# Optimization experiments

Hardware: AMD Instinct MI355X
Metric: run time of the kernel (lower is better)

Reference implementation:

```python
import jax, jax.numpy as jnp
import numpy as np

EMBED_DIM = 1024


def setup_inputs() -> dict:
    key = jax.random.key(0)
    ks = jax.random.split(key, 7)
    B, S, D = 4, 2048, EMBED_DIM
    scale = 1.0 / np.sqrt(D)
    x = jax.random.normal(ks[0], (B, S, D), dtype=jnp.float32)
    # nn.Linear weights stored as [out, in]; we keep [in, out] for x @ W
    Wq = jax.random.normal(ks[1], (D, D), dtype=jnp.float32) * scale
    bq = jax.random.normal(ks[2], (D,), dtype=jnp.float32) * scale
    Wk = jax.random.normal(ks[3], (D, D), dtype=jnp.float32) * scale
    bk = jax.random.normal(ks[4], (D,), dtype=jnp.float32) * scale
    Wv = jax.random.normal(ks[5], (D, D), dtype=jnp.float32) * scale
    bv = jax.random.normal(ks[6], (D,), dtype=jnp.float32) * scale
    return {"x": x, "Wq": Wq, "bq": bq, "Wk": Wk, "bk": bk, "Wv": Wv, "bv": bv}


def reference(x, Wq, bq, Wk, bk, Wv, bv):
    # Single-head attention (num_heads unused in original module).
    q = x @ Wq + bq            # [B, S, D]
    k = x @ Wk + bk            # [B, S, D]
    v = x @ Wv + bv            # [B, S, D]
    inv_sqrt_d = 1.0 / jnp.sqrt(jnp.asarray(x.shape[-1], x.dtype))
    scores = jnp.einsum("bsd,btd->bst", q, k) * inv_sqrt_d  # [B, S, S]
    attn = jax.nn.softmax(scores, axis=-1)
    return jnp.einsum("bst,btd->bsd", attn, v)
```

## Files before the change

kernel.cpp:

```cpp
#include <hip/hip_runtime.h>
#include <hip/hip_bf16.h>


using floatx4 = __attribute__((ext_vector_type(4))) float;
using shortx8 = __attribute__((ext_vector_type(8))) short;
using shortx4 = __attribute__((ext_vector_type(4))) short;

__device__ __forceinline__ short f2bf(float f) {
    __hip_bfloat16 h = __float2bfloat16(f);
    return *reinterpret_cast<short*>(&h);
}
__device__ __forceinline__ float bf2f(short s) {
    unsigned u = (unsigned)(unsigned short)s << 16;
    return __uint_as_float(u);
}

#define MFMA16(a, b, c) __builtin_amdgcn_mfma_f32_16x16x32_bf16((a), (b), (c), 0, 0, 0)

__device__ __forceinline__ void gld_lds16(const void* g, void* l) {
    __builtin_amdgcn_global_load_lds(
        (const __attribute__((address_space(1))) void*)g,
        (__attribute__((address_space(3))) void*)l, 16, 0, 0);
}

__device__ __forceinline__ void gemm_loop(
    const short* __restrict__ A, const short* __restrict__ B,
    size_t lda, size_t ldb, int K,
    short* as_, short* bs_, floatx4 (&acc)[4][4], int w, int l)
{
    const int lr8 = l >> 3;
    const int swz = ((l & 7) ^ lr8) * 8;
    const int lrow = l & 15, quad = l >> 4;
    const int wr = w >> 1, wc = w & 1;
    const int r8r = lrow & 7;
    const short* pa = A + (size_t)(w * 32 + lr8) * lda + swz;
    const short* pb = B + (size_t)(w * 32 + lr8) * ldb + swz;
    short* la = as_ + w * 4 * 512;
    short* lb = bs_ + w * 4 * 512;

    for (int kt = 0; kt < K; kt += 64) {
        for (int c = 0; c < 4; ++c) {
            gld_lds16(pa + (size_t)c * 8 * lda + kt, la + c * 512);
            gld_lds16(pb + (size_t)c * 8 * ldb + kt, lb + c * 512);
        }
        __syncthreads();
        for (int kk = 0; kk < 64; kk += 32) {
            const int xoff = (((kk >> 3) + quad) ^ r8r) << 3;
            shortx8 af[4], bfr[4];
            for (int i = 0; i < 4; ++i)
                af[i] = *reinterpret_cast<const shortx8*>(
                    &as_[(size_t)(wr * 64 + i * 16 + lrow) * 64 + xoff]);
            for (int j = 0; j < 4; ++j)
                bfr[j] = *reinterpret_cast<const shortx8*>(
                    &bs_[(size_t)(wc * 64 + j * 16 + lrow) * 64 + xoff]);
            for (int i = 0; i < 4; ++i)
                for (int j = 0; j < 4; ++j)
                    acc[i][j] = MFMA16(af[i], bfr[j], acc[i][j]);
        }
        __syncthreads();
    }
}

__global__ __launch_bounds__(256) void wconv_kernel(
    const float* __restrict__ Wq, const float* __restrict__ Wk,
    const float* __restrict__ Wv, short* __restrict__ Wt)
{
    const float* src = (blockIdx.z == 0) ? Wq : (blockIdx.z == 1) ? Wk : Wv;
    short* dst = Wt + (size_t)blockIdx.z * 1024 * 1024;
    __shared__ float t[64][65];
    const int k0 = blockIdx.x * 64, n0 = blockIdx.y * 64;
    for (int i = threadIdx.x; i < 64 * 64; i += 256) {
        int r = i >> 6, c = i & 63;
        t[r][c] = src[(size_t)(k0 + r) * 1024 + n0 + c];
    }
    __syncthreads();
    for (int i = threadIdx.x; i < 64 * 64; i += 256) {
        int r = i >> 6, c = i & 63;
        dst[(size_t)(n0 + r) * 1024 + k0 + c] = f2bf(t[c][r]);
    }
}

__global__ __launch_bounds__(256) void xconv_kernel(
    const float* __restrict__ X, short* __restrict__ Xb)
{
    size_t i = ((size_t)blockIdx.x * 256 + threadIdx.x) * 8;
    float4 v0 = *reinterpret_cast<const float4*>(X + i);
    float4 v1 = *reinterpret_cast<const float4*>(X + i + 4);
    shortx8 s;
    s[0] = f2bf(v0.x); s[1] = f2bf(v0.y); s[2] = f2bf(v0.z); s[3] = f2bf(v0.w);
    s[4] = f2bf(v1.x); s[5] = f2bf(v1.y); s[6] = f2bf(v1.z); s[7] = f2bf(v1.w);
    *reinterpret_cast<shortx8*>(Xb + i) = s;
}

__global__ __launch_bounds__(256) void qkv_lds_kernel(
    const short* __restrict__ Xb, const short* __restrict__ Wt,
    const float* __restrict__ bias, short* __restrict__ outN,
    short* __restrict__ outVt, int vmode)
{
    __shared__ short as_[128 * 64];
    __shared__ short bs_[128 * 64];
    const int t = threadIdx.x, w = t >> 6, l = t & 63;
    const int m0 = blockIdx.x * 128, n0 = blockIdx.y * 128;
    const int wr = w >> 1, wc = w & 1, lrow = l & 15, quad = l >> 4;

    floatx4 acc[4][4];
    for (int i = 0; i < 4; ++i)
        for (int j = 0; j < 4; ++j) acc[i][j] = floatx4{0.f, 0.f, 0.f, 0.f};

    gemm_loop(Xb + (size_t)m0 * 1024, Wt + (size_t)n0 * 1024,
              1024, 1024, 1024, as_, bs_, acc, w, l);

    for (int i = 0; i < 4; ++i) {
        int rbase = m0 + wr * 64 + i * 16 + quad * 4;
        for (int j = 0; j < 4; ++j) {
            int col = n0 + wc * 64 + j * 16 + lrow;
            float bv = bias[col];
            if (!vmode) {
                for (int r = 0; r < 4; ++r)
                    outN[(size_t)(rbase + r) * 1024 + col] = f2bf(acc[i][j][r] + bv);
            } else {
                int b = rbase >> 11, sl = rbase & 2047;
                shortx4 s;
                for (int r = 0; r < 4; ++r) s[r] = f2bf(acc[i][j][r] + bv);
                *reinterpret_cast<shortx4*>(&outVt[((size_t)b * 1024 + col) * 2048 + sl]) = s;
            }
        }
    }
}

__global__ __launch_bounds__(256) void qkv_cvt_kernel(
    const float* __restrict__ X, const short* __restrict__ Wt,
    const float* __restrict__ bias, short* __restrict__ outN,
    short* __restrict__ outVt, int vmode)
{
    __shared__ short as_[128 * 64];
    __shared__ short bs_[128 * 64];
    const int t = threadIdx.x, w = t >> 6, l = t & 63;
    const int m0 = blockIdx.x * 128, n0 = blockIdx.y * 128;
    const int wr = w >> 1, wc = w & 1, lrow = l & 15, quad = l >> 4;
    const int r8r = lrow & 7;
    const int lr8 = l >> 3;
    const int swz = ((l & 7) ^ lr8) * 8;
    const short* pb = Wt + (size_t)(n0 + w * 32 + lr8) * 1024 + swz;
    short* lb = bs_ + w * 4 * 512;

    floatx4 acc[4][4];
    for (int i = 0; i < 4; ++i)
        for (int j = 0; j < 4; ++j) acc[i][j] = floatx4{0.f, 0.f, 0.f, 0.f};

    for (int kt = 0; kt < 1024; kt += 64) {
        for (int c = 0; c < 4; ++c)
            gld_lds16(pb + (size_t)c * 8 * 1024 + kt, lb + c * 512);
        for (int i = 0; i < 8; ++i) {
            int fid = t + i * 256;
            int r = fid >> 4, c4 = fid & 15;
            float4 v = *reinterpret_cast<const float4*>(
                &X[(size_t)(m0 + r) * 1024 + kt + c4 * 4]);
            shortx4 s;
            s[0] = f2bf(v.x); s[1] = f2bf(v.y); s[2] = f2bf(v.z); s[3] = f2bf(v.w);
            int pos = ((((c4 >> 1) ^ (r & 7)) << 3) | ((c4 & 1) << 2));
            *reinterpret_cast<shortx4*>(&as_[(size_t)r * 64 + pos]) = s;
        }
        __syncthreads();
        for (int kk = 0; kk < 64; kk += 32) {
            const int xoff = (((kk >> 3) + quad) ^ r8r) << 3;
            shortx8 af[4], bfr[4];
            for (int i = 0; i < 4; ++i)
                af[i] = *reinterpret_cast<const shortx8*>(
                    &as_[(size_t)(wr * 64 + i * 16 + lrow) * 64 + xoff]);
            for (int j = 0; j < 4; ++j)
                bfr[j] = *reinterpret_cast<const shortx8*>(
                    &bs_[(size_t)(wc * 64 + j * 16 + lrow) * 64 + xoff]);
            for (int i = 0; i < 4; ++i)
                for (int j = 0; j < 4; ++j)
                    acc[i][j] = MFMA16(af[i], bfr[j], acc[i][j]);
        }
        __syncthreads();
    }

    for (int i = 0; i < 4; ++i) {
        int rbase = m0 + wr * 64 + i * 16 + quad * 4;
        for (int j = 0; j < 4; ++j) {
            int col = n0 + wc * 64 + j * 16 + lrow;
            float bv = bias[col];
            if (!vmode) {
                for (int r = 0; r < 4; ++r)
                    outN[(size_t)(rbase + r) * 1024 + col] = f2bf(acc[i][j][r] + bv);
            } else {
                int b = rbase >> 11, sl = rbase & 2047;
                shortx4 s;
                for (int r = 0; r < 4; ++r) s[r] = f2bf(acc[i][j][r] + bv);
                *reinterpret_cast<shortx4*>(&outVt[((size_t)b * 1024 + col) * 2048 + sl]) = s;
            }
        }
    }
}

__global__ __launch_bounds__(256) void scores_kernel(
    const short* __restrict__ Qb, const short* __restrict__ Kb,
    short* __restrict__ P, int row_start)
{
    __shared__ short as_[128 * 64];
    __shared__ short bs_[128 * 64];
    const int t = threadIdx.x, w = t >> 6, l = t & 63;
    const int m0 = blockIdx.x * 128;
    const int n0 = blockIdx.y * 128;
    const int g0 = row_start + m0;
    const int b = g0 >> 11;
    const int wr = w >> 1, wc = w & 1, lrow = l & 15, quad = l >> 4;

    floatx4 acc[4][4];
    for (int i = 0; i < 4; ++i)
        for (int j = 0; j < 4; ++j) acc[i][j] = floatx4{0.f, 0.f, 0.f, 0.f};

    gemm_loop(Qb + (size_t)g0 * 1024, Kb + ((size_t)b * 2048 + n0) * 1024,
              1024, 1024, 1024, as_, bs_, acc, w, l);

    for (int i = 0; i < 4; ++i) {
        int rbase = m0 + wr * 64 + i * 16 + quad * 4;
        for (int j = 0; j < 4; ++j) {
            int col = n0 + wc * 64 + j * 16 + lrow;
            for (int r = 0; r < 4; ++r)
                P[(size_t)(rbase + r) * 2048 + col] =
                    f2bf(__expf(acc[i][j][r] * 0.03125f - 20.0f));
        }
    }
}

__global__ __launch_bounds__(256) void rsum_kernel(
    const short* __restrict__ P, float* __restrict__ invs)
{
    const int w = threadIdx.x >> 6, l = threadIdx.x & 63;
    const int row = blockIdx.x * 4 + w;
    const short* pr = P + (size_t)row * 2048;
    float s = 0.f;
    for (int i = 0; i < 4; ++i) {
        shortx8 v = *reinterpret_cast<const shortx8*>(pr + l * 8 + i * 512);
        for (int j = 0; j < 8; ++j) s += bf2f(v[j]);
    }
    for (int m = 32; m >= 1; m >>= 1) s += __shfl_xor(s, m, 64);
    if (l == 0) invs[row] = 1.0f / s;
}

__global__ __launch_bounds__(256) void pv_kernel(
    const short* __restrict__ Pb, const short* __restrict__ Vt,
    const float* __restrict__ invs, float* __restrict__ Out, int row_start)
{
    __shared__ short as_[128 * 64];
    __shared__ short bs_[128 * 64];
    const int t = threadIdx.x, w = t >> 6, l = t & 63;
    const int m0 = blockIdx.x * 128;
    const int n0 = blockIdx.y * 128;
    const int g0 = row_start + m0;
    const int b = g0 >> 11;
    const int wr = w >> 1, wc = w & 1, lrow = l & 15, quad = l >> 4;

    floatx4 acc[4][4];
    for (int i = 0; i < 4; ++i)
        for (int j = 0; j < 4; ++j) acc[i][j] = floatx4{0.f, 0.f, 0.f, 0.f};

    gemm_loop(Pb + (size_t)m0 * 2048, Vt + ((size_t)b * 1024 + n0) * 2048,
              2048, 2048, 2048, as_, bs_, acc, w, l);

    for (int i = 0; i < 4; ++i) {
        int rloc = m0 + wr * 64 + i * 16 + quad * 4;
        int rglb = row_start + rloc;
        float is[4];
        for (int r = 0; r < 4; ++r) is[r] = invs[rloc + r];
        for (int j = 0; j < 4; ++j) {
            int col = n0 + wc * 64 + j * 16 + lrow;
            for (int r = 0; r < 4; ++r)
                Out[(size_t)(rglb + r) * 1024 + col] = acc[i][j][r] * is[r];
        }
    }
}

extern "C" void kernel_launch(void* const* d_in, const int* in_sizes, int n_in,
                              void* d_out, int out_size, void* d_ws, size_t ws_size,
                              hipStream_t stream)
{
    const float* x  = (const float*)d_in[0];
    const float* Wq = (const float*)d_in[1];
    const float* bq = (const float*)d_in[2];
    const float* Wk = (const float*)d_in[3];
    const float* bk = (const float*)d_in[4];
    const float* Wv = (const float*)d_in[5];
    const float* bv = (const float*)d_in[6];
    float* out = (float*)d_out;

    char* ws = (char*)d_ws;
    const size_t WT_B  = (size_t)3 * 1024 * 1024 * 2;
    const size_t QKV_B = (size_t)8192 * 1024 * 2;
    short* Wt = (short*)ws;
    short* Qb = (short*)(ws + WT_B);
    short* Kb = (short*)(ws + WT_B + QKV_B);
    short* Vt = (short*)(ws + WT_B + 2 * QKV_B);
    char*  region = ws + WT_B + 3 * QKV_B;
    const size_t base = WT_B + 3 * QKV_B;

    size_t avail = ws_size > base ? ws_size - base : 0;
    long rows_fit = (long)(avail / (size_t)(2048 * 2 + 4));
    int chunk = (int)(rows_fit & ~127L);
    if (chunk > 8192) chunk = 8192;
    if (chunk < 128) chunk = 128;
    const bool use_xb = avail >= QKV_B;

    short* Pbuf = (short*)region;
    float* invs = (float*)(region + (size_t)chunk * 2048 * 2);

    wconv_kernel<<<dim3(16, 16, 3), 256, 0, stream>>>(Wq, Wk, Wv, Wt);
    if (use_xb) {
        short* Xb = (short*)region;
        xconv_kernel<<<dim3(4096), 256, 0, stream>>>(x, Xb);
        qkv_lds_kernel<<<dim3(64, 8), 256, 0, stream>>>(Xb, Wt,                   bq, Qb, nullptr, 0);
        qkv_lds_kernel<<<dim3(64, 8), 256, 0, stream>>>(Xb, Wt + 1024 * 1024,     bk, Kb, nullptr, 0);
        qkv_lds_kernel<<<dim3(64, 8), 256, 0, stream>>>(Xb, Wt + 2 * 1024 * 1024, bv, nullptr, Vt, 1);
    } else {
        qkv_cvt_kernel<<<dim3(64, 8), 256, 0, stream>>>(x, Wt,                    bq, Qb, nullptr, 0);
        qkv_cvt_kernel<<<dim3(64, 8), 256, 0, stream>>>(x, Wt + 1024 * 1024,      bk, Kb, nullptr, 0);
        qkv_cvt_kernel<<<dim3(64, 8), 256, 0, stream>>>(x, Wt + 2 * 1024 * 1024,  bv, nullptr, Vt, 1);
    }

    for (int rs = 0; rs < 8192; rs += chunk) {
        int rows = 8192 - rs;
        if (rows > chunk) rows = chunk;
        scores_kernel<<<dim3(rows / 128, 16), 256, 0, stream>>>(Qb, Kb, Pbuf, rs);
        rsum_kernel<<<dim3(rows / 4), 256, 0, stream>>>(Pbuf, invs);
        pv_kernel<<<dim3(rows / 128, 8), 256, 0, stream>>>(Pbuf, Vt, invs, out, rs);
    }
}
```

Baseline: 258.0 us.

## Fuse prep and QKV launches, fold softmax row sums into scores kernel

The weight-transpose, x-conversion, bias-concat and sum-zeroing kernels become one prep launch, and the three QKV GEMMs become a single launch over a concatenated N dimension. The separate row-sum kernel is removed: the scores kernel reduces each row's exp values with wave shuffles and accumulates them into a global sums array with atomics. Q and K are now stored in the output buffer to free workspace, and the grid axes are swapped so blocks sharing a row tile are adjacent. This removes several launches and one full re-read of P. In exchange it adds atomic traffic, and it risks corrupting results when chunking overwrites Q and K in the output before later chunks read them.

```diff
diff --git a/kernel.cpp b/kernel.cpp
--- a/kernel.cpp
+++ b/kernel.cpp
@@ -61,47 +61,62 @@
     }
 }
 
-__global__ __launch_bounds__(256) void wconv_kernel(
+__global__ __launch_bounds__(256) void prep_kernel(
+    const float* __restrict__ X,
     const float* __restrict__ Wq, const float* __restrict__ Wk,
-    const float* __restrict__ Wv, short* __restrict__ Wt)
-{
-    const float* src = (blockIdx.z == 0) ? Wq : (blockIdx.z == 1) ? Wk : Wv;
-    short* dst = Wt + (size_t)blockIdx.z * 1024 * 1024;
-    __shared__ float t[64][65];
-    const int k0 = blockIdx.x * 64, n0 = blockIdx.y * 64;
-    for (int i = threadIdx.x; i < 64 * 64; i += 256) {
-        int r = i >> 6, c = i & 63;
-        t[r][c] = src[(size_t)(k0 + r) * 1024 + n0 + c];
-    }
-    __syncthreads();
-    for (int i = threadIdx.x; i < 64 * 64; i += 256) {
-        int r = i >> 6, c = i & 63;
-        dst[(size_t)(n0 + r) * 1024 + k0 + c] = f2bf(t[c][r]);
-    }
-}
-
-__global__ __launch_bounds__(256) void xconv_kernel(
-    const float* __restrict__ X, short* __restrict__ Xb)
-{
-    size_t i = ((size_t)blockIdx.x * 256 + threadIdx.x) * 8;
-    float4 v0 = *reinterpret_cast<const float4*>(X + i);
-    float4 v1 = *reinterpret_cast<const float4*>(X + i + 4);
-    shortx8 s;
-    s[0] = f2bf(v0.x); s[1] = f2bf(v0.y); s[2] = f2bf(v0.z); s[3] = f2bf(v0.w);
-    s[4] = f2bf(v1.x); s[5] = f2bf(v1.y); s[6] = f2bf(v1.z); s[7] = f2bf(v1.w);
-    *reinterpret_cast<shortx8*>(Xb + i) = s;
-}
-
-__global__ __launch_bounds__(256) void qkv_lds_kernel(
+    const float* __restrict__ Wv,
+    const float* __restrict__ bq, const float* __restrict__ bk,
+    const float* __restrict__ bv,
+    short* __restrict__ Xb, short* __restrict__ Wt,
+    float* __restrict__ bcat, float* __restrict__ sums)
+{
+    const int id = blockIdx.x, t = threadIdx.x;
+    if (id < 4096) {
+        size_t i = ((size_t)id * 256 + t) * 8;
+        float4 v0 = *reinterpret_cast<const float4*>(X + i);
+        float4 v1 = *reinterpret_cast<const float4*>(X + i + 4);
+        shortx8 s;
+        s[0] = f2bf(v0.x); s[1] = f2bf(v0.y); s[2] = f2bf(v0.z); s[3] = f2bf(v0.w);
+        s[4] = f2bf(v1.x); s[5] = f2bf(v1.y); s[6] = f2bf(v1.z); s[7] = f2bf(v1.w);
+        *reinterpret_cast<shortx8*>(Xb + i) = s;
+    } else if (id < 4864) {
+        __shared__ float tl[64][65];
+        const int wid = id - 4096;
+        const int z = wid >> 8, t16 = wid & 255;
+        const float* src = (z == 0) ? Wq : (z == 1) ? Wk : Wv;
+        short* dst = Wt + (size_t)z * 1024 * 1024;
+        const int k0 = (t16 >> 4) * 64, n0 = (t16 & 15) * 64;
+        for (int i = t; i < 64 * 64; i += 256) {
+            int r = i >> 6, c = i & 63;
+            tl[r][c] = src[(size_t)(k0 + r) * 1024 + n0 + c];
+        }
+        __syncthreads();
+        for (int i = t; i < 64 * 64; i += 256) {
+            int r = i >> 6, c = i & 63;
+            dst[(size_t)(n0 + r) * 1024 + k0 + c] = f2bf(tl[c][r]);
+        }
+    } else if (id < 4867) {
+        const int z = id - 4864;
+        const float* bsrc = (z == 0) ? bq : (z == 1) ? bk : bv;
+        for (int i = t; i < 1024; i += 256) bcat[z * 1024 + i] = bsrc[i];
+    } else {
+        const int sid = id - 4867;
+        *reinterpret_cast<float4*>(&sums[sid * 1024 + t * 4]) =
+            float4{0.f, 0.f, 0.f, 0.f};
+    }
+}
+
+__global__ __launch_bounds__(256) void qkv_kernel(
     const short* __restrict__ Xb, const short* __restrict__ Wt,
-    const float* __restrict__ bias, short* __restrict__ outN,
-    short* __restrict__ outVt, int vmode)
+    const float* __restrict__ bcat, short* __restrict__ dQ,
+    short* __restrict__ dK, short* __restrict__ Vt)
 {
     __shared__ short as_[128 * 64];
     __shared__ short bs_[128 * 64];
     const int t = threadIdx.x, w = t >> 6, l = t & 63;
-    const int m0 = blockIdx.x * 128, n0 = blockIdx.y * 128;
+    const int n0 = blockIdx.x * 128, m0 = blockIdx.y * 128;
     const int wr = w >> 1, wc = w & 1, lrow = l & 15, quad = l >> 4;
+    const int sec = n0 >> 10;
 
     floatx4 acc[4][4];
     for (int i = 0; i < 4; ++i)
@@ -110,101 +125,75 @@
     gemm_loop(Xb + (size_t)m0 * 1024, Wt + (size_t)n0 * 1024,
               1024, 1024, 1024, as_, bs_, acc, w, l);
 
+    short* outN = (sec == 0) ? dQ : dK;
     for (int i = 0; i < 4; ++i) {
         int rbase = m0 + wr * 64 + i * 16 + quad * 4;
         for (int j = 0; j < 4; ++j) {
-            int col = n0 + wc * 64 + j * 16 + lrow;
-            float bv = bias[col];
-            if (!vmode) {
+            int coln = n0 + wc * 64 + j * 16 + lrow;
+            int col = coln & 1023;
+            float bv = bcat[coln];
+            if (sec < 2) {
                 for (int r = 0; r < 4; ++r)
                     outN[(size_t)(rbase + r) * 1024 + col] = f2bf(acc[i][j][r] + bv);
             } else {
                 int b = rbase >> 11, sl = rbase & 2047;
                 shortx4 s;
                 for (int r = 0; r < 4; ++r) s[r] = f2bf(acc[i][j][r] + bv);
-                *reinterpret_cast<shortx4*>(&outVt[((size_t)b * 1024 + col) * 2048 + sl]) = s;
+                *reinterpret_cast<shortx4*>(&Vt[((size_t)b * 1024 + col) * 2048 + sl]) = s;
             }
         }
     }
 }
 
-__global__ __launch_bounds__(256) void qkv_cvt_kernel(
-    const float* __restrict__ X, const short* __restrict__ Wt,
-    const float* __restrict__ bias, short* __restrict__ outN,
-    short* __restrict__ outVt, int vmode)
+__global__ __launch_bounds__(256) void scores_kernel(
+    const short* __restrict__ dQ, const short* __restrict__ dK,
+    short* __restrict__ P, float* __restrict__ sums, int row_start)
 {
     __shared__ short as_[128 * 64];
     __shared__ short bs_[128 * 64];
     const int t = threadIdx.x, w = t >> 6, l = t & 63;
-    const int m0 = blockIdx.x * 128, n0 = blockIdx.y * 128;
+    const int n0 = blockIdx.x * 128;
+    const int m0 = blockIdx.y * 128;
+    const int g0 = row_start + m0;
+    const int b = g0 >> 11;
     const int wr = w >> 1, wc = w & 1, lrow = l & 15, quad = l >> 4;
-    const int r8r = lrow & 7;
-    const int lr8 = l >> 3;
-    const int swz = ((l & 7) ^ lr8) * 8;
-    const short* pb = Wt + (size_t)(n0 + w * 32 + lr8) * 1024 + swz;
-    short* lb = bs_ + w * 4 * 512;
 
     floatx4 acc[4][4];
     for (int i = 0; i < 4; ++i)
         for (int j = 0; j < 4; ++j) acc[i][j] = floatx4{0.f, 0.f, 0.f, 0.f};
 
-    for (int kt = 0; kt < 1024; kt += 64) {
-        for (int c = 0; c < 4; ++c)
-            gld_lds16(pb + (size_t)c * 8 * 1024 + kt, lb + c * 512);
-        for (int i = 0; i < 8; ++i) {
-            int fid = t + i * 256;
-            int r = fid >> 4, c4 = fid & 15;
-            float4 v = *reinterpret_cast<const float4*>(
-                &X[(size_t)(m0 + r) * 1024 + kt + c4 * 4]);
-            shortx4 s;
-            s[0] = f2bf(v.x); s[1] = f2bf(v.y); s[2] = f2bf(v.z); s[3] = f2bf(v.w);
-            int pos = ((((c4 >> 1) ^ (r & 7)) << 3) | ((c4 & 1) << 2));
-            *reinterpret_cast<shortx4*>(&as_[(size_t)r * 64 + pos]) = s;
-        }
-        __syncthreads();
-        for (int kk = 0; kk < 64; kk += 32) {
-            const int xoff = (((kk >> 3) + quad) ^ r8r) << 3;
-            shortx8 af[4], bfr[4];
-            for (int i = 0; i < 4; ++i)
-                af[i] = *reinterpret_cast<const shortx8*>(
-                    &as_[(size_t)(wr * 64 + i * 16 + lrow) * 64 + xoff]);
-            for (int j = 0; j < 4; ++j)
-                bfr[j] = *reinterpret_cast<const shortx8*>(
-                    &bs_[(size_t)(wc * 64 + j * 16 + lrow) * 64 + xoff]);
-            for (int i = 0; i < 4; ++i)
-                for (int j = 0; j < 4; ++j)
-                    acc[i][j] = MFMA16(af[i], bfr[j], acc[i][j]);
-        }
-        __syncthreads();
-    }
+    gemm_loop(dQ + (size_t)g0 * 1024, dK + ((size_t)b * 2048 + n0) * 1024,
+              1024, 1024, 1024, as_, bs_, acc, w, l);
 
     for (int i = 0; i < 4; ++i) {
-        int rbase = m0 + wr * 64 + i * 16 + quad * 4;
+        int rloc = m0 + wr * 64 + i * 16 + quad * 4;
+        float rs[4] = {0.f, 0.f, 0.f, 0.f};
         for (int j = 0; j < 4; ++j) {
             int col = n0 + wc * 64 + j * 16 + lrow;
-            float bv = bias[col];
-            if (!vmode) {
-                for (int r = 0; r < 4; ++r)
-                    outN[(size_t)(rbase + r) * 1024 + col] = f2bf(acc[i][j][r] + bv);
-            } else {
-                int b = rbase >> 11, sl = rbase & 2047;
-                shortx4 s;
-                for (int r = 0; r < 4; ++r) s[r] = f2bf(acc[i][j][r] + bv);
-                *reinterpret_cast<shortx4*>(&outVt[((size_t)b * 1024 + col) * 2048 + sl]) = s;
+            for (int r = 0; r < 4; ++r) {
+                short pb = f2bf(__expf(acc[i][j][r] * 0.03125f - 20.0f));
+                P[(size_t)(rloc + r) * 2048 + col] = pb;
+                rs[r] += bf2f(pb);
             }
         }
-    }
-}
-
-__global__ __launch_bounds__(256) void scores_kernel(
-    const short* __restrict__ Qb, const short* __restrict__ Kb,
-    short* __restrict__ P, int row_start)
+        for (int r = 0; r < 4; ++r)
+            for (int m = 1; m <= 8; m <<= 1)
+                rs[r] += __shfl_xor(rs[r], m, 64);
+        if (lrow == 0)
+            for (int r = 0; r < 4; ++r)
+                atomicAdd(&sums[row_start + rloc + r], rs[r]);
+    }
+}
+
+__global__ __launch_bounds__(256) void pv_kernel(
+    const short* __restrict__ P, const short* __restrict__ Vt,
+    const float* __restrict__ sums, float* __restrict__ Out, int row_start)
 {
     __shared__ short as_[128 * 64];
     __shared__ short bs_[128 * 64];
     const int t = threadIdx.x, w = t >> 6, l = t & 63;
-    const int m0 = blockIdx.x * 128;
-    const int n0 = blockIdx.y * 128;
+    const int n0 = blockIdx.x * 128;
+    const int m0 = blockIdx.y * 128;
     const int g0 = row_start + m0;
     const int b = g0 >> 11;
     const int wr = w >> 1, wc = w & 1, lrow = l & 15, quad = l >> 4;
@@ -213,60 +202,14 @@
     for (int i = 0; i < 4; ++i)
         for (int j = 0; j < 4; ++j) acc[i][j] = floatx4{0.f, 0.f, 0.f, 0.f};
 
-    gemm_loop(Qb + (size_t)g0 * 1024, Kb + ((size_t)b * 2048 + n0) * 1024,
-              1024, 1024, 1024, as_, bs_, acc, w, l);
-
-    for (int i = 0; i < 4; ++i) {
-        int rbase = m0 + wr * 64 + i * 16 + quad * 4;
-        for (int j = 0; j < 4; ++j) {
-            int col = n0 + wc * 64 + j * 16 + lrow;
-            for (int r = 0; r < 4; ++r)
-                P[(size_t)(rbase + r) * 2048 + col] =
-                    f2bf(__expf(acc[i][j][r] * 0.03125f - 20.0f));
-        }
-    }
-}
-
-__global__ __launch_bounds__(256) void rsum_kernel(
-    const short* __restrict__ P, float* __restrict__ invs)
-{
-    const int w = threadIdx.x >> 6, l = threadIdx.x & 63;
-    const int row = blockIdx.x * 4 + w;
-    const short* pr = P + (size_t)row * 2048;
-    float s = 0.f;
-    for (int i = 0; i < 4; ++i) {
-        shortx8 v = *reinterpret_cast<const shortx8*>(pr + l * 8 + i * 512);
-        for (int j = 0; j < 8; ++j) s += bf2f(v[j]);
-    }
-    for (int m = 32; m >= 1; m >>= 1) s += __shfl_xor(s, m, 64);
-    if (l == 0) invs[row] = 1.0f / s;
-}
-
-__global__ __launch_bounds__(256) void pv_kernel(
-    const short* __restrict__ Pb, const short* __restrict__ Vt,
-    const float* __restrict__ invs, float* __restrict__ Out, int row_start)
-{
-    __shared__ short as_[128 * 64];
-    __shared__ short bs_[128 * 64];
-    const int t = threadIdx.x, w = t >> 6, l = t & 63;
-    const int m0 = blockIdx.x * 128;
-    const int n0 = blockIdx.y * 128;
-    const int g0 = row_start + m0;
-    const int b = g0 >> 11;
-    const int wr = w >> 1, wc = w & 1, lrow = l & 15, quad = l >> 4;
-
-    floatx4 acc[4][4];
-    for (int i = 0; i < 4; ++i)
-        for (int j = 0; j < 4; ++j) acc[i][j] = floatx4{0.f, 0.f, 0.f, 0.f};
-
-    gemm_loop(Pb + (size_t)m0 * 2048, Vt + ((size_t)b * 1024 + n0) * 2048,
+    gemm_loop(P + (size_t)m0 * 2048, Vt + ((size_t)b * 1024 + n0) * 2048,
               2048, 2048, 2048, as_, bs_, acc, w, l);
 
     for (int i = 0; i < 4; ++i) {
         int rloc = m0 + wr * 64 + i * 16 + quad * 4;
         int rglb = row_start + rloc;
         float is[4];
-        for (int r = 0; r < 4; ++r) is[r] = invs[rloc + r];
+        for (int r = 0; r < 4; ++r) is[r] = 1.0f / sums[rglb + r];
         for (int j = 0; j < 4; ++j) {
             int col = n0 + wc * 64 + j * 16 + lrow;
             for (int r = 0; r < 4; ++r)
@@ -288,44 +231,33 @@
     const float* bv = (const float*)d_in[6];
     float* out = (float*)d_out;
 
+    short* dQ = (short*)d_out;
+    short* dK = dQ + (size_t)8192 * 1024;
+
     char* ws = (char*)d_ws;
-    const size_t WT_B  = (size_t)3 * 1024 * 1024 * 2;
-    const size_t QKV_B = (size_t)8192 * 1024 * 2;
-    short* Wt = (short*)ws;
-    short* Qb = (short*)(ws + WT_B);
-    short* Kb = (short*)(ws + WT_B + QKV_B);
-    short* Vt = (short*)(ws + WT_B + 2 * QKV_B);
-    char*  region = ws + WT_B + 3 * QKV_B;
-    const size_t base = WT_B + 3 * QKV_B;
+    short* Wt   = (short*)ws;
+    float* bcat = (float*)(ws + 6291456);
+    float* sums = (float*)(ws + 6291456 + 12288);
+    short* Vt   = (short*)(ws + 6291456 + 12288 + 32768);
+    char*  region = ws + 6291456 + 12288 + 32768 + 16777216;
+    const size_t base = 6291456 + 12288 + 32768 + 16777216;
 
     size_t avail = ws_size > base ? ws_size - base : 0;
-    long rows_fit = (long)(avail / (size_t)(2048 * 2 + 4));
+    long rows_fit = (long)(avail / 4096);
     int chunk = (int)(rows_fit & ~127L);
     if (chunk > 8192) chunk = 8192;
     if (chunk < 128) chunk = 128;
-    const bool use_xb = avail >= QKV_B;
-
-    short* Pbuf = (short*)region;
-    float* invs = (float*)(region + (size_t)chunk * 2048 * 2);
-
-    wconv_kernel<<<dim3(16, 16, 3), 256, 0, stream>>>(Wq, Wk, Wv, Wt);
-    if (use_xb) {
-        short* Xb = (short*)region;
-        xconv_kernel<<<dim3(4096), 256, 0, stream>>>(x, Xb);
-        qkv_lds_kernel<<<dim3(64, 8), 256, 0, stream>>>(Xb, Wt,                   bq, Qb, nullptr, 0);
-        qkv_lds_kernel<<<dim3(64, 8), 256, 0, stream>>>(Xb, Wt + 1024 * 1024,     bk, Kb, nullptr, 0);
-        qkv_lds_kernel<<<dim3(64, 8), 256, 0, stream>>>(Xb, Wt + 2 * 1024 * 1024, bv, nullptr, Vt, 1);
-    } else {
-        qkv_cvt_kernel<<<dim3(64, 8), 256, 0, stream>>>(x, Wt,                    bq, Qb, nullptr, 0);
-        qkv_cvt_kernel<<<dim3(64, 8), 256, 0, stream>>>(x, Wt + 1024 * 1024,      bk, Kb, nullptr, 0);
-        qkv_cvt_kernel<<<dim3(64, 8), 256, 0, stream>>>(x, Wt + 2 * 1024 * 1024,  bv, nullptr, Vt, 1);
-    }
+    short* Xb = (short*)region;
+    short* P  = (short*)region;
+
+    prep_kernel<<<dim3(4875), 256, 0, stream>>>(x, Wq, Wk, Wv, bq, bk, bv,
+                                                Xb, Wt, bcat, sums);
+    qkv_kernel<<<dim3(24, 64), 256, 0, stream>>>(Xb, Wt, bcat, dQ, dK, Vt);
 
     for (int rs = 0; rs < 8192; rs += chunk) {
         int rows = 8192 - rs;
         if (rows > chunk) rows = chunk;
-        scores_kernel<<<dim3(rows / 128, 16), 256, 0, stream>>>(Qb, Kb, Pbuf, rs);
-        rsum_kernel<<<dim3(rows / 4), 256, 0, stream>>>(Pbuf, invs);
-        pv_kernel<<<dim3(rows / 128, 8), 256, 0, stream>>>(Pbuf, Vt, invs, out, rs);
-    }
-}
+        scores_kernel<<<dim3(16, rows / 128), 256, 0, stream>>>(dQ, dK, P, sums, rs);
+        pv_kernel<<<dim3(8, rows / 128), 256, 0, stream>>>(P, Vt, sums, out, rs);
+    }
+}
```

After: 254.4 us. About the same (-1.4%).
